# Performance work log

Measured on AMD Instinct MI355X. Metric: run time of the kernel, lower is better.

The kernel has to match this reference:

```python
import math
import jax, jax.numpy as jnp
import numpy as np

PE_DIM = 128
NUM_HEADS = 8
U = V = 2
TEMP = 10000.0


def sine_pe(y_embed, x_embed, num_pos_feats, temperature, card):
    """Matches get_sine_position_encoding with use_norm=True."""
    eps = 1e-6
    scale = 2.0 * math.pi
    y = y_embed / (card[0] + eps) * scale
    x = x_embed / (card[1] + eps) * scale
    dim_t = jnp.asarray(temperature, jnp.float32) ** (
        2.0 * (jnp.arange(num_pos_feats, dtype=jnp.float32) // 2) / num_pos_feats)
    px = x[..., None] / dim_t
    py = y[..., None] / dim_t

    def interleave(p):
        s = jnp.sin(p[..., 0::2])
        c = jnp.cos(p[..., 1::2])
        return jnp.stack((s, c), axis=-1).reshape(p.shape[:-1] + (-1,))

    return jnp.concatenate((interleave(py), interleave(px)), axis=-1)


def setup_inputs() -> dict:
    key = jax.random.key(0)
    ks = jax.random.split(key, 8)
    B, C, H, W = 2, 64, 256, 256
    dim = C
    # xavier-ish scale for Linear(128 -> 64)
    w_std = math.sqrt(2.0 / (PE_DIM + dim))
    return {
        "feat_supp": jax.random.normal(ks[0], (B, C, H, W), jnp.float32),
        "flow": jax.random.normal(ks[1], (B, H, W, 2), jnp.float32) * 3.0,
        "feat_curr": jax.random.normal(ks[2], (B, C, H, W), jnp.float32),
        "q_w": jax.random.normal(ks[3], (dim, PE_DIM), jnp.float32) * w_std,
        "q_b": jnp.zeros((dim,), jnp.float32),
        "k_w": jax.random.normal(ks[4], (dim, PE_DIM), jnp.float32) * w_std,
        "k_b": jnp.zeros((dim,), jnp.float32),
        "v_w": jax.random.normal(ks[5], (dim, PE_DIM), jnp.float32) * w_std,
        "v_b": jnp.zeros((dim,), jnp.float32),
    }


def reference(feat_supp, flow, feat_curr, q_w, q_b, k_w, k_b, v_w, v_b):
    B, C, H, W = feat_curr.shape
    UV = U * V
    HW = H * W
    nh = NUM_HEADS
    hd = C // nh
    d = PE_DIM // C  # pe channels per feature channel
    scale = hd ** (-0.5)

    # flow-displaced integer grid + fractional part
    img_off = jnp.stack(
        jnp.meshgrid(jnp.arange(H), jnp.arange(W), indexing="ij"), axis=-1
    ).astype(flow.dtype)                                   # (H, W, 2) in (y, x)
    grid_full = img_off[None] + flow[..., ::-1]            # flow flipped to (y, x)
    grid_intg = jnp.floor(grid_full).astype(jnp.int32)
    grid_deci = grid_full - grid_intg                      # (B, H, W, 2)

    win_off = jnp.stack(
        jnp.meshgrid(jnp.arange(U), jnp.arange(V), indexing="ij"), axis=-1
    ).astype(jnp.int32)                                    # (U, V, 2)
    grid_w = grid_intg[:, :, :, None, None, :] + win_off[None, None, None]
    grid_w = grid_w.reshape(B, HW * UV, 2)
    deci = grid_deci.reshape(B, HW, 2)

    # duplicate-padding gather of support features
    h_idx = jnp.clip(grid_w[..., 0], 0, H - 1)
    w_idx = jnp.clip(grid_w[..., 1], 0, W - 1)
    lin = h_idx * W + w_idx                                # (B, HW*UV)
    feat_warp = jnp.take_along_axis(
        feat_supp.reshape(B, C, HW), lin[:, None, :], axis=2)  # (B, C, HW*UV)
    feat_warp = feat_warp.transpose(0, 2, 1).reshape(B, HW, UV, C)

    # window position bias (card = window_size - 1, use_corrected_card=False)
    wy, wx = jnp.meshgrid(jnp.arange(U, dtype=jnp.float32),
                          jnp.arange(V, dtype=jnp.float32), indexing="ij")
    pos_bias = sine_pe(wy.reshape(1, -1), wx.reshape(1, -1),
                       PE_DIM // 2, TEMP, (U - 1, V - 1))   # (1, UV, PE_DIM)
    pe_warp = pos_bias.reshape(1, 1, UV, C, d)
    fw = (feat_warp[..., None] + pe_warp).reshape(B, HW, UV, PE_DIM)

    # current-frame features + fractional-offset positional encoding
    fc = feat_curr.reshape(B, C, HW).transpose(0, 2, 1)     # (B, HW, C)
    pe_curr = sine_pe(deci[..., 0], deci[..., 1],
                      PE_DIM // 2, TEMP, (U, V))            # (B, HW, PE_DIM)
    fc = (fc[..., None] + pe_curr.reshape(B, HW, C, d)).reshape(B, HW, PE_DIM)

    q = (fc @ q_w.T + q_b).reshape(B, HW, nh, hd)
    k = (fw @ k_w.T + k_b).reshape(B, HW, UV, nh, hd)
    v = (fw @ v_w.T + v_b).reshape(B, HW, UV, nh, hd)

    attn = jnp.einsum("bnhd,bnuhd->bnhu", q * scale, k)
    attn = jax.nn.softmax(attn, axis=-1)
    out = jnp.einsum("bnhu,bnuhd->bnhd", attn, v).reshape(B, HW, C)
    return out.reshape(B, H, W, C).transpose(0, 3, 1, 2)
```

## Files before the change

### kernel.cpp

```cpp
#include <hip/hip_runtime.h>
#include <hip/hip_bf16.h>

#define HWHW 65536
#define LN1E4_32 0.28782313662425572f
#define TWO_PI_N 6.2831847f

typedef __attribute__((ext_vector_type(8))) short short8;
typedef __attribute__((ext_vector_type(4))) short s16x4;
typedef __attribute__((ext_vector_type(4))) float f32x4;

#if __has_builtin(__builtin_amdgcn_sinf) && __has_builtin(__builtin_amdgcn_cosf)
#define FSIN(x) __builtin_amdgcn_sinf(x)
#define FCOS(x) __builtin_amdgcn_cosf(x)
#else
#define FSIN(x) __sinf((x) * 6.2831853071795864f)
#define FCOS(x) __cosf((x) * 6.2831853071795864f)
#endif


__device__ __forceinline__ short f2bf(float f) {
  union { __hip_bfloat16 h; short s; } u;
  u.h = __float2bfloat16(f);
  return u.s;
}

__global__ __launch_bounds__(256)
void pre_pass(const float* __restrict__ supp,
              const float* __restrict__ qw, const float* __restrict__ kw,
              const float* __restrict__ vw,
              const float* __restrict__ kb, const float* __restrict__ vb,
              __hip_bfloat16* __restrict__ suppT,
              __hip_bfloat16* __restrict__ wfrag, float* __restrict__ bias) {
  const int t = threadIdx.x;
  if (blockIdx.x < 2048) {
    __shared__ short tile[64 * 68];
    const int b   = blockIdx.x >> 10;
    const int p0  = (blockIdx.x & 1023) << 6;
    const int px4 = (t & 15) << 2;
    const int g   = t >> 4;

    const float* src = supp + ((size_t)b * 64 + g * 4) * HWHW + p0 + px4;
    f32x4 v[4];
#pragma unroll
    for (int c = 0; c < 4; ++c)
      v[c] = *(const f32x4*)(src + (size_t)c * HWHW);
#pragma unroll
    for (int j = 0; j < 4; ++j) {
      s16x4 pk;
#pragma unroll
      for (int c = 0; c < 4; ++c) pk[c] = f2bf(v[c][j]);
      *(s16x4*)&tile[(px4 + j) * 68 + g * 4] = pk;
    }
    __syncthreads();
    const int px = t >> 2, ch0 = (t & 3) << 4;
    s16x4 r0 = *(s16x4*)&tile[px * 68 + ch0];
    s16x4 r1 = *(s16x4*)&tile[px * 68 + ch0 + 4];
    s16x4 r2 = *(s16x4*)&tile[px * 68 + ch0 + 8];
    s16x4 r3 = *(s16x4*)&tile[px * 68 + ch0 + 12];
    short8 o0, o1;
#pragma unroll
    for (int j = 0; j < 4; ++j) {
      o0[j] = r0[j]; o0[j + 4] = r1[j];
      o1[j] = r2[j]; o1[j + 4] = r3[j];
    }
    short8* dst = (short8*)(suppT + ((size_t)(b * HWHW + p0 + px)) * 64 + ch0);
    dst[0] = o0;
    dst[1] = o1;
  } else if (blockIdx.x < 2056) {
    int slot = (blockIdx.x - 2048) * 256 + t;
    __hip_bfloat16* dst = wfrag + slot * 8;
    if (slot < 1024) {
      int ksnt = slot >> 6, lane = slot & 63;
      int ks = ksnt >> 2, nt = ksnt & 3;
      const float* w = qw + (nt * 16 + (lane & 15)) * 128 + ks * 32 + (lane >> 4) * 8;
#pragma unroll
      for (int j = 0; j < 8; ++j) dst[j] = __float2bfloat16(w[j]);
    } else {
      int mat = (slot >= 1536);
      int rem = slot & 511;
      int ksnt = rem >> 6, lane = rem & 63;
      int ks = ksnt >> 2, nt = ksnt & 3;
      int c0 = ks * 32 + (lane >> 4) * 8;
      const float* w = (mat ? vw : kw) + (nt * 16 + (lane & 15)) * 128;
#pragma unroll
      for (int j = 0; j < 8; ++j)
        dst[j] = __float2bfloat16(w[2 * (c0 + j)] + w[2 * (c0 + j) + 1]);
    }
  } else {
    for (int s = t; s < 512; s += 256) {
      int mat = s >> 8, uv = (s >> 6) & 3, c = s & 63;
      const float* w = (mat ? vw : kw) + c * 128;
      float acc = (mat ? vb : kb)[c];
      for (int kk = 0; kk < 128; ++kk) {
        float val = (kk < 64 ? (float)(uv >> 1) : (float)(uv & 1)) * TWO_PI_N;
        int i = kk & 63, f = i >> 1;
        float arg = val * __expf(-(float)f * LN1E4_32);
        float pe = (i & 1) ? __cosf(arg) : __sinf(arg);
        acc += pe * w[kk];
      }
      bias[s] = acc;
    }
  }
}

__global__ __attribute__((amdgpu_waves_per_eu(4, 4))) __launch_bounds__(256)
void iw_main(const __hip_bfloat16* __restrict__ suppT, const float* __restrict__ flow,
             const float* __restrict__ feat_curr,
             const short8* __restrict__ wg, const float* __restrict__ bias_g,
             const float* __restrict__ q_b, float* __restrict__ out)
{
  __shared__ __align__(16) char smem[35072];
  short8* lds_kv   = (short8*)smem;
  f32x4*  lds_bias = (f32x4*)(smem + 16384);
  short8* lds_qw   = (short8*)(smem + 18432);
  float*  outstage = (float*)(smem + 18432);

  const int tid = threadIdx.x;
  const int idx = ((blockIdx.x & 7) << 8) | (blockIdx.x >> 3);
  const int b   = idx >> 10;
  const int hw0 = (idx & 1023) << 6;
  const int lane = tid & 63, wv = tid >> 6;
  const int quad = lane >> 4, l15 = lane & 15;
  const int uvl  = l15 & 3;
  const int prow = l15 >> 2;
  const short8* sT = (const short8*)suppT;

#pragma unroll
  for (int j = 0; j < 4; ++j) {
    lds_qw[j * 256 + tid] = wg[j * 256 + tid];
    lds_kv[j * 256 + tid] = wg[1024 + j * 256 + tid];
  }
  {
    float* bl = (float*)lds_bias;
#pragma unroll
    for (int s_ = 0; s_ < 2; ++s_) {
      int s = s_ * 256 + tid;
      int mat = s >> 8, rem = s & 255, r = rem >> 6, c = rem & 63;
      bl[mat * 256 + (c >> 4) * 64 + (c & 15) * 4 + r] = bias_g[s];
    }
  }
  __syncthreads();

  float invd[2][4];
#pragma unroll
  for (int a = 0; a < 2; ++a)
#pragma unroll
    for (int jj = 0; jj < 4; ++jj)
      invd[a][jj] = __expf(-(float)(a * 16 + quad * 4 + jj) * LN1E4_32);

  int iy, ix;
  f32x4 qacc[4];

  {
    const int qpix = hw0 + wv * 16 + l15;
    float2 fl = ((const float2*)flow)[b * HWHW + qpix];
    float gy = (float)(qpix >> 8) + fl.y;
    float gx = (float)(qpix & 255) + fl.x;
    float fy = floorf(gy), fx = floorf(gx);
    iy = (int)fy; ix = (int)fx;
    float vy = (gy - fy) * 0.49999975f;
    float vx = (gx - fx) * 0.49999975f;

    short8 qa[4];
#pragma unroll
    for (int ks = 0; ks < 4; ++ks) {
      float val = (ks < 2) ? vy : vx;
#pragma unroll
      for (int jj = 0; jj < 4; ++jj) {
        int c = ks * 16 + quad * 4 + jj;
        float feat = feat_curr[(b * 64 + c) * HWHW + qpix];
        float rev = val * invd[ks & 1][jj];
        qa[ks][jj * 2]     = f2bf(feat + FSIN(rev));
        qa[ks][jj * 2 + 1] = f2bf(feat + FCOS(rev));
      }
    }
#pragma unroll
    for (int nt = 0; nt < 4; ++nt) qacc[nt] = (f32x4){0.f, 0.f, 0.f, 0.f};
#pragma unroll
    for (int ks = 0; ks < 4; ++ks)
#pragma unroll
      for (int nt = 0; nt < 4; ++nt)
        qacc[nt] = __builtin_amdgcn_mfma_f32_16x16x32_bf16(
            qa[ks], lds_qw[(ks * 4 + nt) * 64 + lane], qacc[nt], 0, 0, 0);
  }

  int off[4];
#pragma unroll
  for (int m = 0; m < 4; ++m) {
    int p  = m * 4 + prow;
    int yy = min(max(__shfl(iy, p) + (uvl >> 1), 0), 255);
    int xx = min(max(__shfl(ix, p) + (uvl & 1), 0), 255);
    off[m] = (b * HWHW + yy * 256 + xx) * 8;
  }

  __syncthreads();

  short8 ka[4][2];
#pragma unroll
  for (int m = 0; m < 4; ++m) {
    ka[m][0] = sT[off[m] + quad];
    ka[m][1] = sT[off[m] + 4 + quad];
  }

  float qT[4][4];
  {
#pragma unroll
    for (int nt = 0; nt < 4; ++nt) {
      float qb = q_b[nt * 16 + l15];
#pragma unroll
      for (int r = 0; r < 4; ++r)
        qacc[nt][r] = (qacc[nt][r] + qb) * 0.35355339059327373f;
    }
#pragma unroll
    for (int mt = 0; mt < 4; ++mt)
#pragma unroll
      for (int nt = 0; nt < 4; ++nt) {
        int src = mt * 16 + l15;
        float v0 = __shfl(qacc[nt][0], src);
        float v1 = __shfl(qacc[nt][1], src);
        float v2 = __shfl(qacc[nt][2], src);
        float v3 = __shfl(qacc[nt][3], src);
        float t0 = (quad & 2) ? v2 : v0;
        float t1 = (quad & 2) ? v3 : v1;
        qT[mt][nt] = (quad & 1) ? t1 : t0;
      }
  }

#pragma unroll
  for (int nt = 0; nt < 4; ++nt) {
    short8 kf0 = lds_kv[nt * 64 + lane];
    short8 kf1 = lds_kv[(4 + nt) * 64 + lane];
    short8 vf0 = lds_kv[(8 + nt) * 64 + lane];
    short8 vf1 = lds_kv[(12 + nt) * 64 + lane];
    f32x4 kb4 = lds_bias[nt * 16 + l15];
    f32x4 vb4 = lds_bias[64 + nt * 16 + l15];

#pragma unroll
    for (int mt = 0; mt < 4; ++mt) {
      f32x4 kacc = kb4;
      f32x4 vacc = vb4;
      kacc = __builtin_amdgcn_mfma_f32_16x16x32_bf16(ka[mt][0], kf0, kacc, 0, 0, 0);
      kacc = __builtin_amdgcn_mfma_f32_16x16x32_bf16(ka[mt][1], kf1, kacc, 0, 0, 0);
      vacc = __builtin_amdgcn_mfma_f32_16x16x32_bf16(ka[mt][0], vf0, vacc, 0, 0, 0);
      vacc = __builtin_amdgcn_mfma_f32_16x16x32_bf16(ka[mt][1], vf1, vacc, 0, 0, 0);

      float lg[4];
#pragma unroll
      for (int r = 0; r < 4; ++r) {
        float p = qT[mt][nt] * kacc[r];
        p += __int_as_float(__builtin_amdgcn_update_dpp(
                 0, __float_as_int(p), 0xB1, 0xf, 0xf, true));
        p += __int_as_float(__builtin_amdgcn_update_dpp(
                 0, __float_as_int(p), 0x4E, 0xf, 0xf, true));
        p += __int_as_float(__builtin_amdgcn_update_dpp(
                 0, __float_as_int(p), 0x141, 0xf, 0xf, true));
        lg[r] = p;
      }
      float e0 = __expf(lg[0]), e1 = __expf(lg[1]);
      float e2 = __expf(lg[2]), e3 = __expf(lg[3]);
      float inv = 1.0f / (e0 + e1 + e2 + e3);
      float o = (e0 * vacc[0] + e1 * vacc[1] + e2 * vacc[2] + e3 * vacc[3]) * inv;
      outstage[(nt * 16 + l15) * 65 + wv * 16 + mt * 4 + quad] = o;
    }
  }

  __syncthreads();
#pragma unroll
  for (int i = 0; i < 16; ++i) {
    int j = i * 256 + tid;
    int c = j >> 6, p = j & 63;
    out[(b * 64 + c) * HWHW + hw0 + p] = outstage[c * 65 + p];
  }
}

extern "C" void kernel_launch(void* const* d_in, const int* in_sizes, int n_in,
                              void* d_out, int out_size, void* d_ws, size_t ws_size,
                              hipStream_t stream) {
  const float* feat_supp = (const float*)d_in[0];
  const float* flow      = (const float*)d_in[1];
  const float* feat_curr = (const float*)d_in[2];
  const float* q_w = (const float*)d_in[3];
  const float* q_b = (const float*)d_in[4];
  const float* k_w = (const float*)d_in[5];
  const float* k_b = (const float*)d_in[6];
  const float* v_w = (const float*)d_in[7];
  const float* v_b = (const float*)d_in[8];
  float* out = (float*)d_out;
  (void)in_sizes; (void)n_in; (void)out_size; (void)ws_size;

  __hip_bfloat16* wfrag = (__hip_bfloat16*)d_ws;
  float* bias           = (float*)((char*)d_ws + 32768);
  __hip_bfloat16* suppT = (__hip_bfloat16*)((char*)d_ws + 65536);

  hipLaunchKernelGGL(pre_pass, dim3(2057), dim3(256), 0, stream,
                     feat_supp, q_w, k_w, v_w, k_b, v_b, suppT, wfrag, bias);
  hipLaunchKernelGGL(iw_main, dim3(2048), dim3(256), 0, stream,
                     suppT, flow, feat_curr, (const short8*)d_ws, bias, q_b, out);
}
```

Before: 146.3 us.

## Permute query pixel mapping to drop Q transpose shuffles and fold scale into weights

Query pixels are assigned to MFMA rows in a permuted order so that the Q accumulator layout already matches the layout the K/V attention loop consumes. This removes the 64 cross-lane shuffles that transposed Q. The attention scale is folded into the bf16 Q weights and the bias initialisation. The gather loads of warped support features are issued before the Q MFMAs so they can overlap with compute. Scaling the weights before bf16 rounding slightly changes numerics.

Result: no change. 145.4 us (-0.6%).

```diff
diff --git a/kernel.cpp b/kernel.cpp
--- a/kernel.cpp
+++ b/kernel.cpp
@@ -74,7 +74,8 @@
       int ks = ksnt >> 2, nt = ksnt & 3;
       const float* w = qw + (nt * 16 + (lane & 15)) * 128 + ks * 32 + (lane >> 4) * 8;
 #pragma unroll
-      for (int j = 0; j < 8; ++j) dst[j] = __float2bfloat16(w[j]);
+      for (int j = 0; j < 8; ++j)
+        dst[j] = __float2bfloat16(w[j] * 0.35355339059327373f);
     } else {
       int mat = (slot >= 1536);
       int rem = slot & 511;
@@ -123,6 +124,7 @@
   const int quad = lane >> 4, l15 = lane & 15;
   const int uvl  = l15 & 3;
   const int prow = l15 >> 2;
+  const int qsel = ((l15 & 3) << 2) | (l15 >> 2);
   const short8* sT = (const short8*)suppT;
 
 #pragma unroll
@@ -148,16 +150,16 @@
     for (int jj = 0; jj < 4; ++jj)
       invd[a][jj] = __expf(-(float)(a * 16 + quad * 4 + jj) * LN1E4_32);
 
-  int iy, ix;
   f32x4 qacc[4];
+  short8 ka[4][2];
 
   {
-    const int qpix = hw0 + wv * 16 + l15;
+    const int qpix = hw0 + wv * 16 + qsel;
     float2 fl = ((const float2*)flow)[b * HWHW + qpix];
     float gy = (float)(qpix >> 8) + fl.y;
     float gx = (float)(qpix & 255) + fl.x;
     float fy = floorf(gy), fx = floorf(gx);
-    iy = (int)fy; ix = (int)fx;
+    int iy = (int)fy, ix = (int)fx;
     float vy = (gy - fy) * 0.49999975f;
     float vx = (gx - fx) * 0.49999975f;
 
@@ -174,8 +176,22 @@
         qa[ks][jj * 2 + 1] = f2bf(feat + FCOS(rev));
       }
     }
-#pragma unroll
-    for (int nt = 0; nt < 4; ++nt) qacc[nt] = (f32x4){0.f, 0.f, 0.f, 0.f};
+
+#pragma unroll
+    for (int m = 0; m < 4; ++m) {
+      int src = prow * 4 + m;
+      int yy = min(max(__shfl(iy, src) + (uvl >> 1), 0), 255);
+      int xx = min(max(__shfl(ix, src) + (uvl & 1), 0), 255);
+      int off = (b * HWHW + yy * 256 + xx) * 8;
+      ka[m][0] = sT[off + quad];
+      ka[m][1] = sT[off + 4 + quad];
+    }
+
+#pragma unroll
+    for (int nt = 0; nt < 4; ++nt) {
+      float qb = q_b[nt * 16 + l15] * 0.35355339059327373f;
+      qacc[nt] = (f32x4){qb, qb, qb, qb};
+    }
 #pragma unroll
     for (int ks = 0; ks < 4; ++ks)
 #pragma unroll
@@ -184,47 +200,7 @@
             qa[ks], lds_qw[(ks * 4 + nt) * 64 + lane], qacc[nt], 0, 0, 0);
   }
 
-  int off[4];
-#pragma unroll
-  for (int m = 0; m < 4; ++m) {
-    int p  = m * 4 + prow;
-    int yy = min(max(__shfl(iy, p) + (uvl >> 1), 0), 255);
-    int xx = min(max(__shfl(ix, p) + (uvl & 1), 0), 255);
-    off[m] = (b * HWHW + yy * 256 + xx) * 8;
-  }
-
   __syncthreads();
-
-  short8 ka[4][2];
-#pragma unroll
-  for (int m = 0; m < 4; ++m) {
-    ka[m][0] = sT[off[m] + quad];
-    ka[m][1] = sT[off[m] + 4 + quad];
-  }
-
-  float qT[4][4];
-  {
-#pragma unroll
-    for (int nt = 0; nt < 4; ++nt) {
-      float qb = q_b[nt * 16 + l15];
-#pragma unroll
-      for (int r = 0; r < 4; ++r)
-        qacc[nt][r] = (qacc[nt][r] + qb) * 0.35355339059327373f;
-    }
-#pragma unroll
-    for (int mt = 0; mt < 4; ++mt)
-#pragma unroll
-      for (int nt = 0; nt < 4; ++nt) {
-        int src = mt * 16 + l15;
-        float v0 = __shfl(qacc[nt][0], src);
-        float v1 = __shfl(qacc[nt][1], src);
-        float v2 = __shfl(qacc[nt][2], src);
-        float v3 = __shfl(qacc[nt][3], src);
-        float t0 = (quad & 2) ? v2 : v0;
-        float t1 = (quad & 2) ? v3 : v1;
-        qT[mt][nt] = (quad & 1) ? t1 : t0;
-      }
-  }
 
 #pragma unroll
   for (int nt = 0; nt < 4; ++nt) {
@@ -247,7 +223,7 @@
       float lg[4];
 #pragma unroll
       for (int r = 0; r < 4; ++r) {
-        float p = qT[mt][nt] * kacc[r];
+        float p = qacc[nt][mt] * kacc[r];
         p += __int_as_float(__builtin_amdgcn_update_dpp(
                  0, __float_as_int(p), 0xB1, 0xf, 0xf, true));
         p += __int_as_float(__builtin_amdgcn_update_dpp(
```
